# Kernel optimization log

Hardware: AMD Instinct MI355X
Metric: run time of the kernel (lower is better)

Reference implementation:

```python
import jax, jax.numpy as jnp
import numpy as np

CORR_THRESHOLD = 0.5
EPS = 1e-12


def setup_inputs() -> dict:
    key = jax.random.key(0)
    # x: [B, N_channels, T] EEG windows
    x = jax.random.normal(key, (128, 64, 30720), dtype=jnp.float32)
    return {"x": x}


def reference(x):
    # Batched Pearson correlation across channels (rows = variables, like np.corrcoef).
    B, N, T = x.shape
    xc = x - jnp.mean(x, axis=-1, keepdims=True)            # center over time
    cov = jnp.einsum("bnt,bmt->bnm", xc, xc)                # [B, N, N] unnormalized
    norms = jnp.sqrt(jnp.einsum("bnt,bnt->bn", xc, xc))     # [B, N] row L2 norms
    corr = cov / (norms[:, :, None] * norms[:, None, :] + EPS)
    # zero diagonal, then threshold on |corr|
    eye = jnp.eye(N, dtype=bool)
    corr = jnp.where(eye[None], 0.0, corr)
    mask = jnp.abs(corr) >= CORR_THRESHOLD
    adj = jnp.where(mask, corr, 0.0)                        # dense masked adjacency [B, N, N]
    # node features are the raw EEG samples (as in the original Data(x=eeg_sample, ...))
    return adj, x
```

## Files before the change

kernel.cpp:

```cpp
#include <hip/hip_runtime.h>
#include <hip/hip_bf16.h>
#include <cstdint>
#include <cstddef>

#define B_   128
#define NCH  64
#define T_   30720
#define EPSF 1e-12f
#define THRF 0.5f

typedef float  f32x4 __attribute__((ext_vector_type(4)));
typedef short  s16x8 __attribute__((ext_vector_type(8)));
typedef unsigned short u16;

#define AS1 __attribute__((address_space(1)))
#define AS3 __attribute__((address_space(3)))

static __device__ __forceinline__ short bf16s(float f) {
    return (short)__builtin_bit_cast(u16, __float2bfloat16(f));
}

__global__ __launch_bounds__(512) void corr_stage1(
    const float* __restrict__ x, float* __restrict__ out_x,
    float* __restrict__ P, float* __restrict__ S,
    int split, int Tc)
{
    __shared__ __align__(16) float lds[2][NCH * 128];

    const int tid  = threadIdx.x;
    const int lane = tid & 63;
    const int w    = tid >> 6;

    const int bid = blockIdx.x;
    const int b   = bid / split;
    const int c   = bid - b * split;

    const size_t base = (size_t)b * ((size_t)NCH * T_) + (size_t)c * Tc;
    const float* xw = x + base;
    float*       ow = out_x + base;

    const int NT = Tc >> 7;

    const int hi = lane >> 5;
    const int sg = lane & 31;

    auto dma = [&](int tile, int buf) {
        #pragma unroll
        for (int i = 0; i < 4; ++i) {
            const int j  = w * 4 + i;
            const int ch = 2 * j + hi;
            const int gg = sg ^ (ch & 7);
            const float* src = xw + (size_t)ch * T_ + (size_t)(tile * 128 + gg * 4);
            float* dst = &lds[buf][j * 256];
            __builtin_amdgcn_global_load_lds((const AS1 void*)src,
                                             (AS3 void*)dst, 16, 0, 0);
        }
    };

    dma(0, 0);
    asm volatile("s_waitcnt vmcnt(0)" ::: "memory");
    __builtin_amdgcn_s_barrier();
    __builtin_amdgcn_sched_barrier(0);

    if (w < 4) {
        float csum[8];
        #pragma unroll
        for (int kk = 0; kk < 8; ++kk) csum[kk] = 0.f;

        for (int t = 0; t < NT; ++t) {
            const int cur = t & 1;
            if (t + 1 < NT) dma(t + 1, cur ^ 1);

            #pragma unroll
            for (int kk = 0; kk < 8; ++kk) {
                const int row = 16 * w + 2 * kk + hi;
                const f32x4 v = *reinterpret_cast<const f32x4*>(
                    &lds[cur][row * 128 + ((sg ^ (row & 7)) << 2)]);
                *reinterpret_cast<f32x4*>(
                    ow + (size_t)row * T_ + (size_t)(t * 128 + sg * 4)) = v;
                csum[kk] += ((v.x + v.y) + (v.z + v.w));
            }

            asm volatile("s_waitcnt vmcnt(8)" ::: "memory");
            __builtin_amdgcn_s_barrier();
            __builtin_amdgcn_sched_barrier(0);
        }

        #pragma unroll
        for (int kk = 0; kk < 8; ++kk) {
            float v = csum[kk];
            v += __shfl_xor(v, 1,  64);
            v += __shfl_xor(v, 2,  64);
            v += __shfl_xor(v, 4,  64);
            v += __shfl_xor(v, 8,  64);
            v += __shfl_xor(v, 16, 64);
            if ((lane & 31) == 0)
                S[(size_t)bid * NCH + 16 * w + 2 * kk + hi] = v;
        }
    } else {
        const int q  = w - 4;
        const int qr = q >> 1, qc = q & 1;
        const int fr = lane & 15;
        const int g8 = lane >> 4;
        const int fs = fr & 7;

        f32x4 acc[2][2];
        #pragma unroll
        for (int rb = 0; rb < 2; ++rb)
            #pragma unroll
            for (int cb = 0; cb < 2; ++cb) acc[rb][cb] = (f32x4)(0.f);

        for (int t = 0; t < NT; ++t) {
            const int cur = t & 1;
            if (t + 1 < NT) dma(t + 1, cur ^ 1);

            #pragma unroll
            for (int ks = 0; ks < 4; ++ks) {
                const int gl = (ks * 8 + 2 * g8) ^ fs;
                const int gh = (ks * 8 + 2 * g8 + 1) ^ fs;
                s16x8 frag[4];
                #pragma unroll
                for (int e = 0; e < 4; ++e) {
                    const int blk = (e < 2) ? (2 * qr + e) : (2 * qc + (e - 2));
                    const int ro  = (blk * 16 + fr) * 128;
                    const f32x4 lo = *reinterpret_cast<const f32x4*>(
                        &lds[cur][ro + (gl << 2)]);
                    const f32x4 hv = *reinterpret_cast<const f32x4*>(
                        &lds[cur][ro + (gh << 2)]);
                    frag[e][0] = bf16s(lo.x); frag[e][1] = bf16s(lo.y);
                    frag[e][2] = bf16s(lo.z); frag[e][3] = bf16s(lo.w);
                    frag[e][4] = bf16s(hv.x); frag[e][5] = bf16s(hv.y);
                    frag[e][6] = bf16s(hv.z); frag[e][7] = bf16s(hv.w);
                }
                #pragma unroll
                for (int rb = 0; rb < 2; ++rb)
                    #pragma unroll
                    for (int cb = 0; cb < 2; ++cb)
                        acc[rb][cb] = __builtin_amdgcn_mfma_f32_16x16x32_bf16(
                            frag[rb], frag[2 + cb], acc[rb][cb], 0, 0, 0);
            }

            asm volatile("s_waitcnt vmcnt(0)" ::: "memory");
            __builtin_amdgcn_s_barrier();
            __builtin_amdgcn_sched_barrier(0);
        }

        float* Pc = P + ((size_t)bid << 12);
        const int prow = (lane >> 4) << 2;
        const int pcol = lane & 15;
        #pragma unroll
        for (int rb = 0; rb < 2; ++rb)
            #pragma unroll
            for (int cb = 0; cb < 2; ++cb)
                #pragma unroll
                for (int reg = 0; reg < 4; ++reg)
                    Pc[((2 * qr + rb) * 16 + prow + reg) * 64
                       + (2 * qc + cb) * 16 + pcol] = acc[rb][cb][reg];
    }
}

__global__ __launch_bounds__(256) void corr_stage2(
    const float* __restrict__ P, const float* __restrict__ S,
    float* __restrict__ adj, int split)
{
    const int idx = blockIdx.x * 256 + threadIdx.x;
    const int b  = idx >> 12;
    const int nm = idx & 4095;
    const int n  = nm >> 6;
    const int m  = nm & 63;

    float G = 0.f, Gnn = 0.f, Gmm = 0.f, Sn = 0.f, Sm = 0.f;
    for (int c = 0; c < split; ++c) {
        const float* Pc = P + ((size_t)(b * split + c) << 12);
        const float* Sc = S + (size_t)(b * split + c) * NCH;
        G   += Pc[nm];
        Gnn += Pc[n * 65];
        Gmm += Pc[m * 65];
        Sn  += Sc[n];
        Sm  += Sc[m];
    }
    const float invT = 1.0f / (float)T_;
    const float cov  = G   - Sn * Sm * invT;
    const float vn   = Gnn - Sn * Sn * invT;
    const float vm   = Gmm - Sm * Sm * invT;
    const float den  = sqrtf(vn) * sqrtf(vm) + EPSF;
    float corr = cov / den;
    if (n == m) corr = 0.f;
    adj[idx] = (fabsf(corr) >= THRF) ? corr : 0.f;
}

extern "C" void kernel_launch(void* const* d_in, const int* in_sizes, int n_in,
                              void* d_out, int out_size, void* d_ws, size_t ws_size,
                              hipStream_t stream)
{
    const float* x   = (const float*)d_in[0];
    float* out   = (float*)d_out;
    float* adj   = out;
    float* out_x = out + (size_t)B_ * NCH * NCH;

    int split = 4;
    while (split > 1 &&
           (size_t)B_ * split * (4096 + NCH) * sizeof(float) > ws_size)
        split >>= 1;

    float* P = (float*)d_ws;
    float* S = P + (size_t)B_ * split * 4096;
    const int Tc = T_ / split;

    corr_stage1<<<dim3(B_ * split), dim3(512), 0, stream>>>(x, out_x, P, S, split, Tc);
    corr_stage2<<<dim3((B_ * 4096) / 256), dim3(256), 0, stream>>>(P, S, adj, split);
}
```

Baseline: 433.2 us.

## Widen time tiles, double block size, split MFMA K across wave groups

Doubles the time-tile width to 256 and the block to 1024 threads with 128KB of dynamic LDS, and halves the time split to 2 chunks per batch. Eight waves now do the copy and row sums, each covering full rows. Eight MFMA waves split the K dimension by parity, and their partial Gram tiles are combined through LDS before the write to the workspace. The aim is more bytes in flight per block and less partial-result traffic into stage 2. The cost is a larger per-block LDS footprint, fewer blocks in the grid, an extra barrier and LDS reduction, and removal of the workspace-size fallback.

```diff
diff --git a/kernel.cpp b/kernel.cpp
--- a/kernel.cpp
+++ b/kernel.cpp
@@ -6,6 +6,7 @@
 #define B_   128
 #define NCH  64
 #define T_   30720
+#define TW   256
 #define EPSF 1e-12f
 #define THRF 0.5f
 
@@ -20,12 +21,12 @@
     return (short)__builtin_bit_cast(u16, __float2bfloat16(f));
 }
 
-__global__ __launch_bounds__(512) void corr_stage1(
+__global__ __launch_bounds__(1024) void corr_stage1(
     const float* __restrict__ x, float* __restrict__ out_x,
     float* __restrict__ P, float* __restrict__ S,
     int split, int Tc)
 {
-    __shared__ __align__(16) float lds[2][NCH * 128];
+    extern __shared__ __align__(16) float lds[];
 
     const int tid  = threadIdx.x;
     const int lane = tid & 63;
@@ -39,19 +40,16 @@
     const float* xw = x + base;
     float*       ow = out_x + base;
 
-    const int NT = Tc >> 7;
-
-    const int hi = lane >> 5;
-    const int sg = lane & 31;
+    const int NT  = Tc / TW;
+    const int BUF = NCH * TW;
 
     auto dma = [&](int tile, int buf) {
         #pragma unroll
         for (int i = 0; i < 4; ++i) {
-            const int j  = w * 4 + i;
-            const int ch = 2 * j + hi;
-            const int gg = sg ^ (ch & 7);
-            const float* src = xw + (size_t)ch * T_ + (size_t)(tile * 128 + gg * 4);
-            float* dst = &lds[buf][j * 256];
+            const int r  = w * 4 + i;
+            const int gg = lane ^ (r & 7);
+            const float* src = xw + (size_t)r * T_ + (size_t)(tile * TW + gg * 4);
+            float* dst = &lds[buf * BUF + r * TW];
             __builtin_amdgcn_global_load_lds((const AS1 void*)src,
                                              (AS3 void*)dst, 16, 0, 0);
         }
@@ -62,23 +60,24 @@
     __builtin_amdgcn_s_barrier();
     __builtin_amdgcn_sched_barrier(0);
 
-    if (w < 4) {
+    if (w < 8) {
         float csum[8];
         #pragma unroll
-        for (int kk = 0; kk < 8; ++kk) csum[kk] = 0.f;
+        for (int i = 0; i < 8; ++i) csum[i] = 0.f;
 
         for (int t = 0; t < NT; ++t) {
             const int cur = t & 1;
             if (t + 1 < NT) dma(t + 1, cur ^ 1);
 
             #pragma unroll
-            for (int kk = 0; kk < 8; ++kk) {
-                const int row = 16 * w + 2 * kk + hi;
+            for (int i = 0; i < 8; ++i) {
+                const int row  = w * 8 + i;
+                const int slot = lane ^ (row & 7);
                 const f32x4 v = *reinterpret_cast<const f32x4*>(
-                    &lds[cur][row * 128 + ((sg ^ (row & 7)) << 2)]);
+                    &lds[cur * BUF + row * TW + slot * 4]);
                 *reinterpret_cast<f32x4*>(
-                    ow + (size_t)row * T_ + (size_t)(t * 128 + sg * 4)) = v;
-                csum[kk] += ((v.x + v.y) + (v.z + v.w));
+                    ow + (size_t)row * T_ + (size_t)(t * TW + lane * 4)) = v;
+                csum[i] += ((v.x + v.y) + (v.z + v.w));
             }
 
             asm volatile("s_waitcnt vmcnt(8)" ::: "memory");
@@ -86,23 +85,28 @@
             __builtin_amdgcn_sched_barrier(0);
         }
 
-        #pragma unroll
-        for (int kk = 0; kk < 8; ++kk) {
-            float v = csum[kk];
+        __syncthreads();
+
+        #pragma unroll
+        for (int i = 0; i < 8; ++i) {
+            float v = csum[i];
             v += __shfl_xor(v, 1,  64);
             v += __shfl_xor(v, 2,  64);
             v += __shfl_xor(v, 4,  64);
             v += __shfl_xor(v, 8,  64);
             v += __shfl_xor(v, 16, 64);
-            if ((lane & 31) == 0)
-                S[(size_t)bid * NCH + 16 * w + 2 * kk + hi] = v;
+            v += __shfl_xor(v, 32, 64);
+            if (lane == 0)
+                S[(size_t)bid * NCH + w * 8 + i] = v;
         }
     } else {
-        const int q  = w - 4;
-        const int qr = q >> 1, qc = q & 1;
-        const int fr = lane & 15;
-        const int g8 = lane >> 4;
-        const int fs = fr & 7;
+        const int g   = w - 8;
+        const int q   = g & 3;
+        const int par = g >> 2;
+        const int qr  = q >> 1, qc = q & 1;
+        const int fr  = lane & 15;
+        const int g8  = lane >> 4;
+        const int fs  = fr & 7;
 
         f32x4 acc[2][2];
         #pragma unroll
@@ -115,18 +119,17 @@
             if (t + 1 < NT) dma(t + 1, cur ^ 1);
 
             #pragma unroll
-            for (int ks = 0; ks < 4; ++ks) {
+            for (int kk = 0; kk < 4; ++kk) {
+                const int ks = par + 2 * kk;
                 const int gl = (ks * 8 + 2 * g8) ^ fs;
                 const int gh = (ks * 8 + 2 * g8 + 1) ^ fs;
                 s16x8 frag[4];
                 #pragma unroll
                 for (int e = 0; e < 4; ++e) {
                     const int blk = (e < 2) ? (2 * qr + e) : (2 * qc + (e - 2));
-                    const int ro  = (blk * 16 + fr) * 128;
-                    const f32x4 lo = *reinterpret_cast<const f32x4*>(
-                        &lds[cur][ro + (gl << 2)]);
-                    const f32x4 hv = *reinterpret_cast<const f32x4*>(
-                        &lds[cur][ro + (gh << 2)]);
+                    const int ro  = cur * BUF + (blk * 16 + fr) * TW;
+                    const f32x4 lo = *reinterpret_cast<const f32x4*>(&lds[ro + gl * 4]);
+                    const f32x4 hv = *reinterpret_cast<const f32x4*>(&lds[ro + gh * 4]);
                     frag[e][0] = bf16s(lo.x); frag[e][1] = bf16s(lo.y);
                     frag[e][2] = bf16s(lo.z); frag[e][3] = bf16s(lo.w);
                     frag[e][4] = bf16s(hv.x); frag[e][5] = bf16s(hv.y);
@@ -145,17 +148,34 @@
             __builtin_amdgcn_sched_barrier(0);
         }
 
-        float* Pc = P + ((size_t)bid << 12);
-        const int prow = (lane >> 4) << 2;
-        const int pcol = lane & 15;
-        #pragma unroll
-        for (int rb = 0; rb < 2; ++rb)
-            #pragma unroll
-            for (int cb = 0; cb < 2; ++cb)
-                #pragma unroll
-                for (int reg = 0; reg < 4; ++reg)
-                    Pc[((2 * qr + rb) * 16 + prow + reg) * 64
-                       + (2 * qc + cb) * 16 + pcol] = acc[rb][cb][reg];
+        if (par == 1) {
+            #pragma unroll
+            for (int rb = 0; rb < 2; ++rb)
+                #pragma unroll
+                for (int cb = 0; cb < 2; ++cb)
+                    #pragma unroll
+                    for (int reg = 0; reg < 4; ++reg)
+                        lds[q * 1024 + lane * 16 + rb * 8 + cb * 4 + reg]
+                            = acc[rb][cb][reg];
+        }
+
+        __syncthreads();
+
+        if (par == 0) {
+            float* Pc = P + ((size_t)bid << 12);
+            const int prow = (lane >> 4) << 2;
+            const int pcol = lane & 15;
+            #pragma unroll
+            for (int rb = 0; rb < 2; ++rb)
+                #pragma unroll
+                for (int cb = 0; cb < 2; ++cb)
+                    #pragma unroll
+                    for (int reg = 0; reg < 4; ++reg)
+                        Pc[((2 * qr + rb) * 16 + prow + reg) * 64
+                           + (2 * qc + cb) * 16 + pcol]
+                            = acc[rb][cb][reg]
+                            + lds[q * 1024 + lane * 16 + rb * 8 + cb * 4 + reg];
+        }
     }
 }
 
@@ -198,15 +218,12 @@
     float* adj   = out;
     float* out_x = out + (size_t)B_ * NCH * NCH;
 
-    int split = 4;
-    while (split > 1 &&
-           (size_t)B_ * split * (4096 + NCH) * sizeof(float) > ws_size)
-        split >>= 1;
-
+    const int split = 2;
     float* P = (float*)d_ws;
     float* S = P + (size_t)B_ * split * 4096;
     const int Tc = T_ / split;
 
-    corr_stage1<<<dim3(B_ * split), dim3(512), 0, stream>>>(x, out_x, P, S, split, Tc);
+    corr_stage1<<<dim3(B_ * split), dim3(1024), 131072, stream>>>(
+        x, out_x, P, S, split, Tc);
     corr_stage2<<<dim3((B_ * 4096) / 256), dim3(256), 0, stream>>>(P, S, adj, split);
 }
```

After: 433.4 us, median of 2. No clear change (+0.1%).
